# Kernel optimization log

Measured on AMD Instinct MI355X. Metric: run time of the kernel, lower is better.

Reference implementation:

```python
import jax, jax.numpy as jnp
import numpy as np

B, N, C, H, W = 64, 500, 256, 64, 64


def grid_sample_bilinear(im, pts):
    """torch.grid_sample bilinear, align_corners=True, padding_mode='zeros'.
    im: [B,C,H,W]; pts: [B,N,2] (x,y) in [-1,1] -> [B,C,N]."""
    b, c, h, w = im.shape
    x = (pts[..., 0] + 1.0) * 0.5 * (w - 1)  # [B,N]
    y = (pts[..., 1] + 1.0) * 0.5 * (h - 1)
    x0 = jnp.floor(x); y0 = jnp.floor(y)
    x1 = x0 + 1.0; y1 = y0 + 1.0
    wx1 = x - x0; wx0 = 1.0 - wx1
    wy1 = y - y0; wy0 = 1.0 - wy1
    flat = im.reshape(b, c, h * w)

    def gather(xi, yi):
        inb = (xi >= 0) & (xi <= w - 1) & (yi >= 0) & (yi <= h - 1)
        xc = jnp.clip(xi, 0, w - 1).astype(jnp.int32)
        yc = jnp.clip(yi, 0, h - 1).astype(jnp.int32)
        idx = (yc * w + xc)[:, None, :]  # [B,1,N]
        g = jnp.take_along_axis(flat, idx, axis=2)  # [B,C,N]
        return g * inb[:, None, :].astype(im.dtype)

    return (gather(x0, y0) * (wx0 * wy0)[:, None, :]
            + gather(x1, y0) * (wx1 * wy0)[:, None, :]
            + gather(x0, y1) * (wx0 * wy1)[:, None, :]
            + gather(x1, y1) * (wx1 * wy1)[:, None, :])


def setup_inputs() -> dict:
    key = jax.random.key(0)
    ks = jax.random.split(key, 12)
    p = jax.random.uniform(ks[0], (B, N, 2), jnp.float32, -1.0, 1.0)
    s_feat = jax.random.normal(ks[1], (B, C, H, W), jnp.float32)
    def conv_p(k, co, ci):
        k1, k2 = jax.random.split(k)
        s = 1.0 / np.sqrt(ci)
        return (jax.random.uniform(k1, (co, ci), jnp.float32, -s, s),
                jax.random.uniform(k2, (co,), jnp.float32, -s, s))
    w0, b0 = conv_p(ks[2], 128, 256)
    w1, b1 = conv_p(ks[3], 64, 128 + 256)
    w2, b2 = conv_p(ks[4], 5, 64 + 256)
    fc_w, fc_b = conv_p(ks[5], 236, 5 * N)
    return {"p": p, "s_feat": s_feat, "w0": w0, "b0": b0, "w1": w1, "b1": b1,
            "w2": w2, "b2": b2, "fc_w": fc_w, "fc_b": fc_b}


def reference(p, s_feat, w0, b0, w1, b1, w2, b2, fc_w, fc_b):
    feat = grid_sample_bilinear(s_feat, p)  # [B,256,N]
    y = jnp.einsum('oc,bcn->bon', w0, feat) + b0[None, :, None]
    y = jax.nn.leaky_relu(y, 0.01)
    y = jnp.einsum('oc,bcn->bon', w1, jnp.concatenate([y, feat], axis=1)) + b1[None, :, None]
    y = jax.nn.leaky_relu(y, 0.01)
    y = jnp.einsum('oc,bcn->bon', w2, jnp.concatenate([y, feat], axis=1)) + b2[None, :, None]
    y = jax.nn.relu(y)           # last_op
    y = y.reshape(y.shape[0], -1)  # [B, 5*N]
    return y @ fc_w.T + fc_b       # [B, 236]
```

## Files before the change

kernel.cpp:

```cpp
#include <hip/hip_runtime.h>
#include <hip/hip_bf16.h>

#define BB 64
#define NN 500
#define CC 256
#define HH 64
#define WW 64
#define HWSZ 4096
#define NPTS 32000
#define NPAD 512

typedef __attribute__((ext_vector_type(4))) short s4v;
typedef __attribute__((ext_vector_type(8))) short s8v;
typedef __attribute__((ext_vector_type(4))) float f4v;
typedef __attribute__((ext_vector_type(4))) int i4v;

__device__ __forceinline__ unsigned short bfround(float f) {
    unsigned u = __builtin_bit_cast(unsigned, f);
    return (unsigned short)((u + 0x7FFFu + ((u >> 16) & 1u)) >> 16);
}

#define GATHER_BLKS 2048
#define NCHB 8
#define NBUF 3
#define W0F_N 32768
#define W1F_N 24576
#define W2F_N 5120
#define PACK_N (W0F_N + W1F_N + W2F_N)
#define FCT_N 590000
#define PACKALL_N (PACK_N + FCT_N)
#define PACK_BLKS ((PACKALL_N + 511) / 512)

__global__ __launch_bounds__(512) void k_gp(const float* __restrict__ sfeat,
                                            const float* __restrict__ pts,
                                            const float* __restrict__ w0,
                                            const float* __restrict__ w1,
                                            const float* __restrict__ w2,
                                            const float* __restrict__ fcw,
                                            unsigned int* __restrict__ featB,
                                            unsigned short* __restrict__ w0f,
                                            unsigned short* __restrict__ w1f,
                                            unsigned short* __restrict__ w2f,
                                            float* __restrict__ fcwT) {
    __shared__ float im[NBUF][HWSZ];
    const int blk = blockIdx.x;
    const int tid = threadIdx.x;

    if (blk >= GATHER_BLKS) {
        int i = (blk - GATHER_BLKS) * 512 + tid;
        if (i < W0F_N) {
            int j = i & 7, ll = (i >> 3) & 63, s = (i >> 9) & 7, m = i >> 12;
            int row = m * 16 + (ll & 15), k = s * 32 + (ll >> 4) * 8 + j;
            w0f[i] = bfround(w0[row * 256 + k]);
        } else if (i < W0F_N + W1F_N) {
            int d = i - W0F_N;
            int j = d & 7, ll = (d >> 3) & 63, rest = d >> 9;
            int s = rest % 12, m = rest / 12;
            int row = m * 16 + (ll & 15), k = s * 32 + (ll >> 4) * 8 + j;
            w1f[d] = bfround(w1[row * 384 + k]);
        } else if (i < PACK_N) {
            int d = i - (W0F_N + W1F_N);
            int j = d & 7, ll = (d >> 3) & 63, s = d >> 9;
            int row = ll & 15, k = s * 32 + (ll >> 4) * 8 + j;
            float v = (row < 5) ? w2[row * 320 + k] : 0.f;
            w2f[d] = bfround(v);
        } else if (i < PACKALL_N) {
            int d = i - PACK_N;
            int k = d / 236, o = d - k * 236;
            fcwT[d] = fcw[o * 2500 + k];
        }
        return;
    }

    const int b     = blk >> 5;
    const int chunk = blk & 31;
    const int ch0   = chunk * NCHB;
    const int n     = tid;

    int4 id = make_int4(0, 0, 0, 0);
    float4 wt = make_float4(0.f, 0.f, 0.f, 0.f);
    if (n < NN) {
        float x = (pts[((size_t)b * NN + n) * 2 + 0] + 1.f) * 0.5f * (float)(WW - 1);
        float y = (pts[((size_t)b * NN + n) * 2 + 1] + 1.f) * 0.5f * (float)(HH - 1);
        float x0f = floorf(x), y0f = floorf(y);
        float x1f = x0f + 1.f, y1f = y0f + 1.f;
        float wx1 = x - x0f, wx0 = 1.f - wx1;
        float wy1 = y - y0f, wy0 = 1.f - wy1;
        float mx0 = (x0f >= 0.f && x0f <= (float)(WW - 1)) ? 1.f : 0.f;
        float mx1 = (x1f >= 0.f && x1f <= (float)(WW - 1)) ? 1.f : 0.f;
        float my0 = (y0f >= 0.f && y0f <= (float)(HH - 1)) ? 1.f : 0.f;
        float my1 = (y1f >= 0.f && y1f <= (float)(HH - 1)) ? 1.f : 0.f;
        int x0 = (int)fminf(fmaxf(x0f, 0.f), (float)(WW - 1));
        int x1 = (int)fminf(fmaxf(x1f, 0.f), (float)(WW - 1));
        int y0 = (int)fminf(fmaxf(y0f, 0.f), (float)(HH - 1));
        int y1 = (int)fminf(fmaxf(y1f, 0.f), (float)(HH - 1));
        id = make_int4(y0 * WW + x0, y0 * WW + x1, y1 * WW + x0, y1 * WW + x1);
        wt = make_float4(wx0 * wy0 * mx0 * my0, wx1 * wy0 * mx1 * my0,
                         wx0 * wy1 * mx0 * my1, wx1 * wy1 * mx1 * my1);
    }

    const float4* src = (const float4*)(sfeat + ((size_t)b * CC + ch0) * HWSZ);

#define ISSUE_CH(T, BUF)                                                      \
    {                                                                         \
        const float4* s2 = src + (size_t)(T) * (HWSZ / 4);                    \
        float4* dst = (float4*)im[BUF];                                       \
        _Pragma("unroll")                                                     \
        for (int it = 0; it < 2; it++) {                                      \
            int j = it * 512 + tid;                                           \
            __builtin_amdgcn_global_load_lds(                                 \
                (const __attribute__((address_space(1))) void*)(s2 + j),      \
                (__attribute__((address_space(3))) void*)(dst + j),           \
                16, 0, 0);                                                    \
        }                                                                     \
    }

    ISSUE_CH(0, 0);
    ISSUE_CH(1, 1);

    unsigned short hprev = 0;
    for (int t = 0; t < NCHB; t++) {
        if (t + 2 < NCHB) {
            ISSUE_CH(t + 2, (t + 2) % 3);
            asm volatile("s_waitcnt vmcnt(4)" ::: "memory");
        } else if (t + 1 < NCHB) {
            asm volatile("s_waitcnt vmcnt(2)" ::: "memory");
        } else {
            asm volatile("s_waitcnt vmcnt(0)" ::: "memory");
        }
        asm volatile("s_barrier" ::: "memory");

        if (n < NN) {
            const float* L = im[t % 3];
            float r = wt.x * L[id.x] + wt.y * L[id.y] + wt.z * L[id.z] + wt.w * L[id.w];
            unsigned short h = bfround(r);
            if (t & 1) {
                unsigned int v = (unsigned int)hprev | ((unsigned int)h << 16);
                featB[(((size_t)b * 32 + chunk) * 4 + (t >> 1)) * 512 + n] = v;
            } else {
                hprev = h;
            }
        }
        if (t + 1 < NCHB)
            asm volatile("s_barrier" ::: "memory");
    }
#undef ISSUE_CH
}

#define K1_S 136
#define K2_S 72

__device__ __forceinline__ s8v mkfrag(const unsigned short* p) {
    return *(const s8v*)p;
}

__global__ __launch_bounds__(512, 4) void k_mlp(const unsigned int* __restrict__ featB,
                                                const unsigned short* __restrict__ w0f,
                                                const unsigned short* __restrict__ w1f,
                                                const unsigned short* __restrict__ w2f,
                                                const float* __restrict__ b0,
                                                const float* __restrict__ b1,
                                                const float* __restrict__ b2,
                                                float* __restrict__ y2f) {
    __shared__ unsigned short c1B[32 * K1_S];
    __shared__ unsigned short c2B[32 * K2_S];

    const int b   = blockIdx.y;
    const int n0  = blockIdx.x * 32;
    const int tid = threadIdx.x;
    const int w   = tid >> 6, l = tid & 63;
    const int nt  = w & 1, mh = w >> 1;
    const int lo16 = l & 15, hi = l >> 4;
    const int c = nt * 16 + lo16;

    s8v bhs[8];
    const unsigned int* fb = featB + (size_t)b * (32 * 4 * 512) + (n0 + c);
#pragma unroll
    for (int s = 0; s < 8; s++) {
        const int kg = s * 4 + hi;
        i4v hx;
#pragma unroll
        for (int t = 0; t < 4; t++)
            hx[t] = (int)fb[(size_t)(kg * 4 + t) * 512];
        bhs[s] = __builtin_bit_cast(s8v, hx);
    }

    f4v acc0 = {0.f, 0.f, 0.f, 0.f}, acc1 = {0.f, 0.f, 0.f, 0.f};
#pragma unroll
    for (int s = 0; s < 8; s++) {
        const s8v a0 = mkfrag(w0f + ((size_t)((mh * 2) * 8 + s) * 64 + l) * 8);
        const s8v a1 = mkfrag(w0f + ((size_t)((mh * 2 + 1) * 8 + s) * 64 + l) * 8);
        acc0 = __builtin_amdgcn_mfma_f32_16x16x32_bf16(a0, bhs[s], acc0, 0, 0, 0);
        acc1 = __builtin_amdgcn_mfma_f32_16x16x32_bf16(a1, bhs[s], acc1, 0, 0, 0);
    }
#pragma unroll
    for (int m = 0; m < 2; m++) {
#pragma unroll
        for (int r = 0; r < 4; r++) {
            int ch = (mh * 2 + m) * 16 + hi * 4 + r;
            float v = (m ? acc1[r] : acc0[r]) + b0[ch];
            v = v > 0.f ? v : 0.01f * v;
            c1B[c * K1_S + ch] = bfround(v);
        }
    }
    __syncthreads();

    f4v accA = {0.f, 0.f, 0.f, 0.f};
#pragma unroll
    for (int s = 0; s < 4; s++) {
        const s8v bh = *(const s8v*)&c1B[c * K1_S + s * 32 + hi * 8];
        const s8v a  = mkfrag(w1f + ((size_t)(mh * 12 + s) * 64 + l) * 8);
        accA = __builtin_amdgcn_mfma_f32_16x16x32_bf16(a, bh, accA, 0, 0, 0);
    }
#pragma unroll
    for (int s = 4; s < 12; s++) {
        const s8v a = mkfrag(w1f + ((size_t)(mh * 12 + s) * 64 + l) * 8);
        accA = __builtin_amdgcn_mfma_f32_16x16x32_bf16(a, bhs[s - 4], accA, 0, 0, 0);
    }
#pragma unroll
    for (int r = 0; r < 4; r++) {
        int ch = mh * 16 + hi * 4 + r;
        float v = accA[r] + b1[ch];
        v = v > 0.f ? v : 0.01f * v;
        c2B[c * K2_S + ch] = bfround(v);
    }
    __syncthreads();

    if (mh == 0) {
        f4v acc2 = {0.f, 0.f, 0.f, 0.f};
#pragma unroll
        for (int s = 0; s < 2; s++) {
            const s8v bh = *(const s8v*)&c2B[c * K2_S + s * 32 + hi * 8];
            const s8v a  = mkfrag(w2f + ((size_t)s * 64 + l) * 8);
            acc2 = __builtin_amdgcn_mfma_f32_16x16x32_bf16(a, bh, acc2, 0, 0, 0);
        }
#pragma unroll
        for (int s = 2; s < 10; s++) {
            const s8v a = mkfrag(w2f + ((size_t)s * 64 + l) * 8);
            acc2 = __builtin_amdgcn_mfma_f32_16x16x32_bf16(a, bhs[s - 2], acc2, 0, 0, 0);
        }
#pragma unroll
        for (int r = 0; r < 4; r++) {
            int ch = hi * 4 + r;
            if (ch < 5) {
                float v = acc2[r] + b2[ch];
                v = fmaxf(v, 0.f);
                int n = n0 + c;
                if (n < NN) y2f[(size_t)b * 2500 + ch * NN + n] = v;
            }
        }
    }
}

__global__ __launch_bounds__(256) void k_fc1(const float* __restrict__ y2f,
                                             const float* __restrict__ fcwT,
                                             float* __restrict__ part) {
    __shared__ float ys[313];
    const int b  = blockIdx.x & 63;
    const int kc = blockIdx.x >> 6;
    const int start = kc * 312 + (kc < 4 ? kc : 4);
    const int len   = (kc < 4) ? 313 : 312;
    const float* yb = y2f + (size_t)b * 2500 + start;
    for (int j = threadIdx.x; j < len; j += 256) ys[j] = yb[j];
    __syncthreads();
    const int o = threadIdx.x;
    if (o < 236) {
        float acc = 0.f;
        const float* wp = fcwT + (size_t)start * 236 + o;
#pragma unroll 8
        for (int k = 0; k < len; k++) acc = fmaf(wp[(size_t)k * 236], ys[k], acc);
        part[((size_t)kc * 64 + b) * 236 + o] = acc;
    }
}

__global__ __launch_bounds__(256) void k_fc2(const float* __restrict__ part,
                                             const float* __restrict__ fcb,
                                             float* __restrict__ out) {
    const int b = blockIdx.x;
    const int o = threadIdx.x;
    if (o < 236) {
        float acc = fcb[o];
#pragma unroll
        for (int kc = 0; kc < 8; kc++) acc += part[((size_t)kc * 64 + b) * 236 + o];
        out[b * 236 + o] = acc;
    }
}

extern "C" void kernel_launch(void* const* d_in, const int* in_sizes, int n_in,
                              void* d_out, int out_size, void* d_ws, size_t ws_size,
                              hipStream_t stream) {
    const float* p   = (const float*)d_in[0];
    const float* sf  = (const float*)d_in[1];
    const float* w0  = (const float*)d_in[2];
    const float* b0  = (const float*)d_in[3];
    const float* w1  = (const float*)d_in[4];
    const float* b1  = (const float*)d_in[5];
    const float* w2  = (const float*)d_in[6];
    const float* b2  = (const float*)d_in[7];
    const float* fcw = (const float*)d_in[8];
    const float* fcb = (const float*)d_in[9];
    float* out = (float*)d_out;

    char* ws = (char*)d_ws;
    unsigned int*   featB = (unsigned int*)(ws);
    float*          y2f   = (float*)(ws + 16777216);
    float*          fcwT  = (float*)(ws + 17417216);
    float*          part  = (float*)(ws + 19777216);
    unsigned short* w0f   = (unsigned short*)(ws + 20260544);
    unsigned short* w1f   = (unsigned short*)(ws + 20326080);
    unsigned short* w2f   = (unsigned short*)(ws + 20375232);

    k_gp<<<GATHER_BLKS + PACK_BLKS, 512, 0, stream>>>(sf, p, w0, w1, w2, fcw,
                                                      featB, w0f, w1f, w2f, fcwT);
    k_mlp<<<dim3(16, BB), 512, 0, stream>>>(featB, w0f, w1f, w2f,
                                            b0, b1, b2, y2f);
    k_fc1<<<512, 256, 0, stream>>>(y2f, fcwT, part);
    k_fc2<<<BB, 256, 0, stream>>>(part, fcb, out);
}
```

Baseline: 82.18 us.

## Tile fc weight transpose through shared memory and widen MLP point tile

The fc weight transpose moves from a strided per-element scatter into dedicated blocks. Each block stages a 64x64 tile in shared memory so that both the reads and the writes are coalesced. Separately, the MLP kernel now handles 64 points per block instead of 32, and each wave computes 4 (layer 0) or 2 (layer 1) output-channel tiles. Each weight fragment load is therefore reused across more MFMAs. This halves the number of MLP blocks, which leaves fewer blocks to spread across the GPU. The extra accumulators and larger shared buffers raise register and LDS use, which may reduce occupancy.

```diff
diff --git a/kernel.cpp b/kernel.cpp
--- a/kernel.cpp
+++ b/kernel.cpp
@@ -27,9 +27,9 @@
 #define W1F_N 24576
 #define W2F_N 5120
 #define PACK_N (W0F_N + W1F_N + W2F_N)
-#define FCT_N 590000
-#define PACKALL_N (PACK_N + FCT_N)
-#define PACK_BLKS ((PACKALL_N + 511) / 512)
+#define PACK_BLKS ((PACK_N + 511) / 512)
+#define TR_BLKS (40 * 4)
+#define TOTAL_BLKS (GATHER_BLKS + PACK_BLKS + TR_BLKS)
 
 __global__ __launch_bounds__(512) void k_gp(const float* __restrict__ sfeat,
                                             const float* __restrict__ pts,
@@ -45,6 +45,25 @@
     __shared__ float im[NBUF][HWSZ];
     const int blk = blockIdx.x;
     const int tid = threadIdx.x;
+
+    if (blk >= GATHER_BLKS + PACK_BLKS) {
+        float (*tile)[65] = (float(*)[65])im;
+        const int tb = blk - (GATHER_BLKS + PACK_BLKS);
+        const int kt = tb % 40, ot = tb / 40;
+        const int k0 = kt * 64, o0 = ot * 64;
+        for (int i = tid; i < 64 * 64; i += 512) {
+            int oo = i >> 6, kk = i & 63;
+            int o = o0 + oo, k = k0 + kk;
+            tile[oo][kk] = (o < 236 && k < 2500) ? fcw[(size_t)o * 2500 + k] : 0.f;
+        }
+        __syncthreads();
+        for (int i = tid; i < 64 * 64; i += 512) {
+            int kk = i >> 6, oo = i & 63;
+            int o = o0 + oo, k = k0 + kk;
+            if (o < 236 && k < 2500) fcwT[(size_t)k * 236 + o] = tile[oo][kk];
+        }
+        return;
+    }
 
     if (blk >= GATHER_BLKS) {
         int i = (blk - GATHER_BLKS) * 512 + tid;
@@ -64,10 +83,6 @@
             int row = ll & 15, k = s * 32 + (ll >> 4) * 8 + j;
             float v = (row < 5) ? w2[row * 320 + k] : 0.f;
             w2f[d] = bfround(v);
-        } else if (i < PACKALL_N) {
-            int d = i - PACK_N;
-            int k = d / 236, o = d - k * 236;
-            fcwT[d] = fcw[o * 2500 + k];
         }
         return;
     }
@@ -162,14 +177,14 @@
                                                 const float* __restrict__ b1,
                                                 const float* __restrict__ b2,
                                                 float* __restrict__ y2f) {
-    __shared__ unsigned short c1B[32 * K1_S];
-    __shared__ unsigned short c2B[32 * K2_S];
+    __shared__ unsigned short c1B[64 * K1_S];
+    __shared__ unsigned short c2B[64 * K2_S];
 
     const int b   = blockIdx.y;
-    const int n0  = blockIdx.x * 32;
+    const int n0  = blockIdx.x * 64;
     const int tid = threadIdx.x;
     const int w   = tid >> 6, l = tid & 63;
-    const int nt  = w & 1, mh = w >> 1;
+    const int nt  = w & 3, mh = w >> 2;
     const int lo16 = l & 15, hi = l >> 4;
     const int c = nt * 16 + lo16;
 
@@ -185,44 +200,58 @@
         bhs[s] = __builtin_bit_cast(s8v, hx);
     }
 
-    f4v acc0 = {0.f, 0.f, 0.f, 0.f}, acc1 = {0.f, 0.f, 0.f, 0.f};
+    f4v acc[4];
+#pragma unroll
+    for (int q = 0; q < 4; q++) acc[q] = (f4v){0.f, 0.f, 0.f, 0.f};
 #pragma unroll
     for (int s = 0; s < 8; s++) {
-        const s8v a0 = mkfrag(w0f + ((size_t)((mh * 2) * 8 + s) * 64 + l) * 8);
-        const s8v a1 = mkfrag(w0f + ((size_t)((mh * 2 + 1) * 8 + s) * 64 + l) * 8);
-        acc0 = __builtin_amdgcn_mfma_f32_16x16x32_bf16(a0, bhs[s], acc0, 0, 0, 0);
-        acc1 = __builtin_amdgcn_mfma_f32_16x16x32_bf16(a1, bhs[s], acc1, 0, 0, 0);
-    }
-#pragma unroll
-    for (int m = 0; m < 2; m++) {
+#pragma unroll
+        for (int q = 0; q < 4; q++) {
+            const s8v a = mkfrag(w0f + ((size_t)((mh * 4 + q) * 8 + s) * 64 + l) * 8);
+            acc[q] = __builtin_amdgcn_mfma_f32_16x16x32_bf16(a, bhs[s], acc[q], 0, 0, 0);
+        }
+    }
+#pragma unroll
+    for (int q = 0; q < 4; q++) {
 #pragma unroll
         for (int r = 0; r < 4; r++) {
-            int ch = (mh * 2 + m) * 16 + hi * 4 + r;
-            float v = (m ? acc1[r] : acc0[r]) + b0[ch];
+            int ch = (mh * 4 + q) * 16 + hi * 4 + r;
+            float v = acc[q][r] + b0[ch];
             v = v > 0.f ? v : 0.01f * v;
             c1B[c * K1_S + ch] = bfround(v);
         }
     }
     __syncthreads();
 
-    f4v accA = {0.f, 0.f, 0.f, 0.f};
+    f4v accA[2];
+#pragma unroll
+    for (int q = 0; q < 2; q++) accA[q] = (f4v){0.f, 0.f, 0.f, 0.f};
 #pragma unroll
     for (int s = 0; s < 4; s++) {
         const s8v bh = *(const s8v*)&c1B[c * K1_S + s * 32 + hi * 8];
-        const s8v a  = mkfrag(w1f + ((size_t)(mh * 12 + s) * 64 + l) * 8);
-        accA = __builtin_amdgcn_mfma_f32_16x16x32_bf16(a, bh, accA, 0, 0, 0);
+#pragma unroll
+        for (int q = 0; q < 2; q++) {
+            const s8v a = mkfrag(w1f + ((size_t)((mh * 2 + q) * 12 + s) * 64 + l) * 8);
+            accA[q] = __builtin_amdgcn_mfma_f32_16x16x32_bf16(a, bh, accA[q], 0, 0, 0);
+        }
     }
 #pragma unroll
     for (int s = 4; s < 12; s++) {
-        const s8v a = mkfrag(w1f + ((size_t)(mh * 12 + s) * 64 + l) * 8);
-        accA = __builtin_amdgcn_mfma_f32_16x16x32_bf16(a, bhs[s - 4], accA, 0, 0, 0);
-    }
-#pragma unroll
-    for (int r = 0; r < 4; r++) {
-        int ch = mh * 16 + hi * 4 + r;
-        float v = accA[r] + b1[ch];
-        v = v > 0.f ? v : 0.01f * v;
-        c2B[c * K2_S + ch] = bfround(v);
+#pragma unroll
+        for (int q = 0; q < 2; q++) {
+            const s8v a = mkfrag(w1f + ((size_t)((mh * 2 + q) * 12 + s) * 64 + l) * 8);
+            accA[q] = __builtin_amdgcn_mfma_f32_16x16x32_bf16(a, bhs[s - 4], accA[q], 0, 0, 0);
+        }
+    }
+#pragma unroll
+    for (int q = 0; q < 2; q++) {
+#pragma unroll
+        for (int r = 0; r < 4; r++) {
+            int ch = (mh * 2 + q) * 16 + hi * 4 + r;
+            float v = accA[q][r] + b1[ch];
+            v = v > 0.f ? v : 0.01f * v;
+            c2B[c * K2_S + ch] = bfround(v);
+        }
     }
     __syncthreads();
 
@@ -310,10 +339,10 @@
     unsigned short* w1f   = (unsigned short*)(ws + 20326080);
     unsigned short* w2f   = (unsigned short*)(ws + 20375232);
 
-    k_gp<<<GATHER_BLKS + PACK_BLKS, 512, 0, stream>>>(sf, p, w0, w1, w2, fcw,
-                                                      featB, w0f, w1f, w2f, fcwT);
-    k_mlp<<<dim3(16, BB), 512, 0, stream>>>(featB, w0f, w1f, w2f,
-                                            b0, b1, b2, y2f);
+    k_gp<<<TOTAL_BLKS, 512, 0, stream>>>(sf, p, w0, w1, w2, fcw,
+                                         featB, w0f, w1f, w2f, fcwT);
+    k_mlp<<<dim3(8, BB), 512, 0, stream>>>(featB, w0f, w1f, w2f,
+                                           b0, b1, b2, y2f);
     k_fc1<<<512, 256, 0, stream>>>(y2f, fcwT, part);
     k_fc2<<<BB, 256, 0, stream>>>(part, fcb, out);
 }
```

After: 79.62 us (median of 3 runs). 3.1% less time.
